# Optimization experiments

Hardware: AMD Instinct MI355X
Metric: run time of the kernel (lower is better)

The kernel has to match this reference:

```python
import jax, jax.numpy as jnp
import numpy as np

N_NODES = 50000
N_EDGES = 1000000
D = 66
NEG_SLOPE = 0.2
EPS_BN = 1e-5


def _glorot(key, shape):
    fan = sum(shape)
    lim = jnp.sqrt(6.0 / fan)
    return jax.random.uniform(key, shape, jnp.float32, -lim, lim)


def setup_inputs() -> dict:
    key = jax.random.key(0)
    ks = jax.random.split(key, 40)
    inp = {
        'h': jax.random.normal(ks[0], (N_NODES, D), jnp.float32),
        'edge_index': jax.random.randint(ks[1], (2, N_EDGES), 0, N_NODES, jnp.int32),
        'edge_weight': jax.random.uniform(ks[2], (N_EDGES, 1), jnp.float32),
        'bn_gamma': jnp.ones((D,), jnp.float32),
        'bn_beta': jnp.zeros((D,), jnp.float32),
    }
    i = 3
    for l in (1, 2, 3):
        inp[f'W{l}'] = _glorot(ks[i], (D, D)); i += 1
        inp[f'b{l}'] = jnp.zeros((D,), jnp.float32)
        inp[f'att_src{l}'] = _glorot(ks[i], (D,)); i += 1
        inp[f'att_dst{l}'] = _glorot(ks[i], (D,)); i += 1
        inp[f'We{l}'] = _glorot(ks[i], (1, D)); i += 1
        inp[f'att_e{l}'] = _glorot(ks[i], (D,)); i += 1
    dims = [(D, D), (D, D), (D, D), (D, D), (D, 22)]
    for l, (din, dout) in enumerate(dims, start=1):
        inp[f'fc{l}_w'] = _glorot(ks[i], (din, dout)); i += 1
        inp[f'fc{l}_b'] = jnp.zeros((dout,), jnp.float32)
    return inp


def _gat_conv(h, src, dst, edge_weight, W, b, att_src, att_dst, We, att_e):
    x = h @ W                                     # [N, D]
    a_src = x @ att_src                           # [N]
    a_dst = x @ att_dst                           # [N]
    a_e = (edge_weight @ We) @ att_e              # [E]
    alpha = a_src[src] + a_dst[dst] + a_e         # [E]
    alpha = jnp.where(alpha > 0, alpha, NEG_SLOPE * alpha)
    # scatter-softmax over destination nodes
    m = jax.ops.segment_max(alpha, dst, num_segments=N_NODES)
    m = jnp.where(jnp.isfinite(m), m, 0.0)
    ex = jnp.exp(alpha - m[dst])
    denom = jax.ops.segment_sum(ex, dst, num_segments=N_NODES)
    coef = ex / (denom[dst] + 1e-16)              # [E]
    out = jax.ops.segment_sum(coef[:, None] * x[src], dst, num_segments=N_NODES)
    return out + b


def reference(h, edge_index, edge_weight, bn_gamma, bn_beta,
              W1, b1, att_src1, att_dst1, We1, att_e1,
              W2, b2, att_src2, att_dst2, We2, att_e2,
              W3, b3, att_src3, att_dst3, We3, att_e3,
              fc1_w, fc1_b, fc2_w, fc2_b, fc3_w, fc3_b,
              fc4_w, fc4_b, fc5_w, fc5_b):
    src, dst = edge_index[0], edge_index[1]
    # BatchNorm1d (training-mode batch statistics, biased variance)
    mean = h.mean(0)
    var = ((h - mean) ** 2).mean(0)
    x = (h - mean) * jax.lax.rsqrt(var + EPS_BN) * bn_gamma + bn_beta
    x = jax.nn.relu(_gat_conv(x, src, dst, edge_weight, W1, b1, att_src1, att_dst1, We1, att_e1))
    x = jax.nn.relu(_gat_conv(x, src, dst, edge_weight, W2, b2, att_src2, att_dst2, We2, att_e2))
    x = jax.nn.relu(_gat_conv(x, src, dst, edge_weight, W3, b3, att_src3, att_dst3, We3, att_e3))
    x = jax.nn.relu(x @ fc1_w + fc1_b)
    x = jax.nn.relu(x @ fc2_w + fc2_b)
    x = jax.nn.relu(x @ fc3_w + fc3_b)
    x = jax.nn.relu(x @ fc4_w + fc4_b)
    return x @ fc5_w + fc5_b
```

## Files before the change

kernel.cpp:

```cpp
#include <hip/hip_runtime.h>
#include <math.h>

#define D 66
#define SP 68
#define NEG_SLOPE 0.2f
#define CAP 6144

typedef short s8v __attribute__((ext_vector_type(8)));
typedef float f4v __attribute__((ext_vector_type(4)));

__device__ __forceinline__ float lrelu(float a){ return a > 0.f ? a : NEG_SLOPE * a; }
__device__ __forceinline__ void fma4(float4& a, float s, const float4& w){
  a.x = fmaf(s, w.x, a.x); a.y = fmaf(s, w.y, a.y);
  a.z = fmaf(s, w.z, a.z); a.w = fmaf(s, w.w, a.w);
}
__device__ __forceinline__ unsigned short bf16r(float f){
  unsigned u = __float_as_uint(f);
  u += 0x7FFFu + ((u >> 16) & 1u);
  return (unsigned short)(u >> 16);
}
__device__ __forceinline__ float bf16f(unsigned short b){
  return __uint_as_float(((unsigned)b) << 16);
}
__device__ __forceinline__ void split8d(const float* p, s8v& a0, s8v& a1){
  #pragma unroll
  for (int j = 0; j < 8; j++){
    float v = p[j];
    unsigned u0 = __float_as_uint(v) & 0xFFFF0000u;
    float r1 = v - __uint_as_float(u0);
    a0[j] = (short)(u0 >> 16);
    a1[j] = (short)(__float_as_uint(r1) >> 16);
  }
}
#define MM4(acc, a0, a1, b0v, b1v)                                         \
  acc = __builtin_amdgcn_mfma_f32_16x16x32_bf16(a0, b0v, acc, 0, 0, 0);    \
  acc = __builtin_amdgcn_mfma_f32_16x16x32_bf16(a1, b0v, acc, 0, 0, 0);    \
  acc = __builtin_amdgcn_mfma_f32_16x16x32_bf16(a0, b1v, acc, 0, 0, 0);    \
  acc = __builtin_amdgcn_mfma_f32_16x16x32_bf16(a1, b1v, acc, 0, 0, 0);

__global__ __launch_bounds__(256) void k_stats_hist(const float* __restrict__ h, const int* __restrict__ dst,
                                                    float* __restrict__ sums, int* __restrict__ bhist,
                                                    int n, int E){
  int t = threadIdx.x;
  if (blockIdx.x < 256){
    __shared__ float ls[2 * D];
    if (t < 2 * D) ls[t] = 0.f;
    __syncthreads();
    int rpb = (n + 255) / 256;
    int r0 = blockIdx.x * rpb;
    int r1 = min(n, r0 + rpb);
    if (t < 3 * D){
      int c = t % D, seg = t / D;
      float s1 = 0.f, s2 = 0.f;
      for (int r = r0 + seg; r < r1; r += 3){
        float v = h[(size_t)r * D + c];
        s1 += v; s2 += v * v;
      }
      atomicAdd(&ls[c], s1);
      atomicAdd(&ls[D + c], s2);
    }
    __syncthreads();
    if (t < 2 * D) atomicAdd(&sums[t], ls[t]);
  } else {
    __shared__ int hh[256];
    hh[t] = 0;
    __syncthreads();
    int stride = 256 * 256;
    for (int e = (blockIdx.x - 256) * 256 + t; e < E; e += stride)
      atomicAdd(&hh[dst[e] >> 8], 1);
    __syncthreads();
    if (hh[t]) atomicAdd(&bhist[t], hh[t]);
  }
}

struct PrepArgs {
  const float *sums, *gamma, *beta;
  const float *We[3], *ae[3];
  const float *gw[3];
  const float *fw[5], *fb[5];
  float *misc; short *W0, *W1; short *F0, *F1; float *bpack;
  int n;
};

__global__ __launch_bounds__(256) void k_prep(PrepArgs pa){
  int t = threadIdx.x;
  if (blockIdx.x == 0){
    if (t < D){
      float mean = pa.sums[t] / (float)pa.n;
      float var  = pa.sums[D + t] / (float)pa.n - mean * mean;
      float inv  = rsqrtf(var + 1e-5f);
      float sc = pa.gamma[t] * inv;
      pa.misc[t] = sc;
      pa.misc[D + t] = pa.beta[t] - mean * sc;
    } else if (t >= D && t < D + 3){
      int l = t - D;
      float c = 0.f;
      for (int d = 0; d < D; d++) c += pa.We[l][d] * pa.ae[l][d];
      pa.misc[2 * D + l] = c;
    }
  } else if (blockIdx.x <= 12){
    int tid = (blockIdx.x - 1) * 256 + t;
    if (tid >= 3 * 960) return;
    int L = tid & 63;
    int ct = (tid >> 6) % 15;
    int lay = tid / 960;
    const float* w = pa.gw[lay];
    int c = ct / 5, tt = ct % 5;
    int nn = tt * 16 + (L & 15);
    int kb = c * 32 + (L >> 4) * 8;
    #pragma unroll
    for (int j = 0; j < 8; j++){
      int k = kb + j;
      float v = (k < D && nn < D) ? w[k * D + nn] : 0.f;
      unsigned short b0 = bf16r(v);
      float r1 = v - bf16f(b0);
      unsigned short b1 = bf16r(r1);
      pa.W0[tid * 8 + j] = (short)b0;
      pa.W1[tid * 8 + j] = (short)b1;
    }
  } else {
    int tid = (blockIdx.x - 13) * 256 + t;
    if (tid < 5 * 960){
      int L = tid & 63;
      int ct = (tid >> 6) % 15;
      int lay = tid / 960;
      const float* w = pa.fw[lay];
      int ncol = (lay == 4) ? 22 : D;
      int c = ct / 5, tt = ct % 5;
      int nn = tt * 16 + (L & 15);
      int kb = c * 32 + (L >> 4) * 8;
      #pragma unroll
      for (int j = 0; j < 8; j++){
        int k = kb + j;
        float v = (k < D && nn < ncol) ? w[k * ncol + nn] : 0.f;
        unsigned short b0 = bf16r(v);
        float r1 = v - bf16f(b0);
        unsigned short b1 = bf16r(r1);
        pa.F0[tid * 8 + j] = (short)b0;
        pa.F1[tid * 8 + j] = (short)b1;
      }
    } else if (tid < 5 * 960 + 400){
      int i = tid - 5 * 960;
      int lay = i / 80, col = i % 80;
      int ncol = (lay == 4) ? 22 : D;
      pa.bpack[i] = (col < ncol) ? pa.fb[lay][col] : 0.f;
    }
  }
}

__global__ void k_bscan(const int* __restrict__ bhist, int* __restrict__ bbase,
                        int* __restrict__ gcur, int* __restrict__ rowptr, int N, int E){
  __shared__ int sh[256];
  int t = threadIdx.x;
  int v = bhist[t];
  sh[t] = v; __syncthreads();
  for (int o = 1; o < 256; o <<= 1){
    int u = (t >= o) ? sh[t - o] : 0;
    __syncthreads();
    sh[t] += u;
    __syncthreads();
  }
  int ex = sh[t] - v;
  bbase[t] = ex;
  gcur[t] = ex;
  if (t == 255){ bbase[256] = sh[255]; rowptr[N] = E; }
}

#define PCHUNK 4096
__global__ __launch_bounds__(256) void k_part(const int* __restrict__ src, const int* __restrict__ dst,
                                              const float* __restrict__ ew,
                                              int* __restrict__ gcur, int2* __restrict__ tmp, int E){
  __shared__ int hist[256];
  __shared__ int base[256];
  int t = threadIdx.x;
  int e0 = blockIdx.x * PCHUNK;
  int eend = min(E, e0 + PCHUNK);
  hist[t] = 0;
  __syncthreads();
  for (int e = e0 + t; e < eend; e += 256)
    atomicAdd(&hist[dst[e] >> 8], 1);
  __syncthreads();
  if (hist[t] > 0) base[t] = atomicAdd(&gcur[t], hist[t]);
  hist[t] = 0;
  __syncthreads();
  for (int e = e0 + t; e < eend; e += 256){
    int d = dst[e];
    int b = d >> 8;
    int off = atomicAdd(&hist[b], 1);
    tmp[base[b] + off] = make_int2((src[e] & 0xffff) | ((d & 255) << 16), __float_as_int(ew[e]));
  }
}

__global__ __launch_bounds__(256) void k_bsort(const int2* __restrict__ tmp, const int* __restrict__ bbase,
                                               int2* __restrict__ epair, int* __restrict__ rowptr, int N){
  __shared__ int2 ebuf[CAP];
  __shared__ int lcnt[256];
  __shared__ int sc[256];
  __shared__ int lcur[256];
  int b = blockIdx.x, t = threadIdx.x;
  int s0 = bbase[b], s1 = bbase[b + 1];
  int cnt = s1 - s0;
  lcnt[t] = 0;
  __syncthreads();
  for (int j = t; j < cnt; j += 256){
    int2 e = tmp[s0 + j];
    if (j < CAP) ebuf[j] = e;
    atomicAdd(&lcnt[(e.x >> 16) & 255], 1);
  }
  __syncthreads();
  int v = lcnt[t];
  sc[t] = v; __syncthreads();
  for (int o = 1; o < 256; o <<= 1){
    int u = (t >= o) ? sc[t - o] : 0;
    __syncthreads();
    sc[t] += u;
    __syncthreads();
  }
  int ex = sc[t] - v;
  int node = (b << 8) + t;
  if (node < N) rowptr[node] = s0 + ex;
  lcur[t] = ex;
  __syncthreads();
  for (int j = t; j < cnt; j += 256){
    int2 e = (j < CAP) ? ebuf[j] : tmp[s0 + j];
    int i = (e.x >> 16) & 255;
    int p = atomicAdd(&lcur[i], 1);
    epair[s0 + p] = make_int2(e.x & 0xffff, e.y);
  }
}

template<bool BN_IN>
__global__ __launch_bounds__(256) void k_mm(const float* __restrict__ X,
    const short* __restrict__ W0, const short* __restrict__ W1,
    const float* __restrict__ att_s, const float* __restrict__ att_d,
    const float* __restrict__ bn,
    float* __restrict__ Y, float* __restrict__ a_src, float* __restrict__ a_dst, int n){
  const int wv = threadIdx.x >> 6, L = threadIdx.x & 63;
  const int quad = L >> 4, m = L & 15;
  const int row0 = blockIdx.x * 64 + wv * 16;
  const int lrow = min(row0 + m, n - 1);
  f4v acc[5];
  #pragma unroll
  for (int t = 0; t < 5; t++) acc[t] = (f4v){0.f,0.f,0.f,0.f};

  #pragma unroll
  for (int c = 0; c < 3; c++){
    float xv[8];
    if (c < 2){
      if (BN_IN){
        const float* hr = X + (size_t)lrow * D + c * 32 + quad * 8;
        #pragma unroll
        for (int j = 0; j < 8; j += 2){
          float2 hv = *(const float2*)(hr + j);
          int col = c * 32 + quad * 8 + j;
          xv[j]     = hv.x * bn[col]     + bn[D + col];
          xv[j + 1] = hv.y * bn[col + 1] + bn[D + col + 1];
        }
      } else {
        const float* xr = X + (size_t)lrow * SP;
        float4 p0 = *(const float4*)&xr[c * 32 + quad * 8];
        float4 p1 = *(const float4*)&xr[c * 32 + quad * 8 + 4];
        xv[0] = p0.x; xv[1] = p0.y; xv[2] = p0.z; xv[3] = p0.w;
        xv[4] = p1.x; xv[5] = p1.y; xv[6] = p1.z; xv[7] = p1.w;
      }
    } else {
      #pragma unroll
      for (int j = 0; j < 8; j++) xv[j] = 0.f;
      if (quad == 0){
        if (BN_IN){
          float2 hv = *(const float2*)(X + (size_t)lrow * D + 64);
          xv[0] = hv.x * bn[64] + bn[D + 64];
          xv[1] = hv.y * bn[65] + bn[D + 65];
        } else {
          float4 p0 = *(const float4*)&X[(size_t)lrow * SP + 64];
          xv[0] = p0.x; xv[1] = p0.y; xv[2] = p0.z; xv[3] = p0.w;
        }
      }
    }
    s8v a0, a1;
    split8d(xv, a0, a1);
    const short* b0p = W0 + (c * 5) * 512 + L * 8;
    const short* b1p = W1 + (c * 5) * 512 + L * 8;
    #pragma unroll
    for (int t = 0; t < 5; t++){
      s8v b0v = *(const s8v*)(b0p + t * 512);
      s8v b1v = *(const s8v*)(b1p + t * 512);
      MM4(acc[t], a0, a1, b0v, b1v)
    }
  }

  float ps[4] = {0.f,0.f,0.f,0.f}, pd[4] = {0.f,0.f,0.f,0.f};
  #pragma unroll
  for (int t = 0; t < 5; t++){
    int col = t * 16 + m;
    float as_v = 0.f, ad_v = 0.f;
    if (col < D){ as_v = att_s[col]; ad_v = att_d[col]; }
    #pragma unroll
    for (int r = 0; r < 4; r++){
      ps[r] += acc[t][r] * as_v;
      pd[r] += acc[t][r] * ad_v;
    }
  }
  #pragma unroll
  for (int r = 0; r < 4; r++){
    int rw = row0 + quad * 4 + r;
    if (rw < n){
      float* yr = Y + (size_t)rw * SP;
      #pragma unroll
      for (int t = 0; t < 4; t++) yr[t * 16 + m] = acc[t][r];
      if (m < 4) yr[64 + m] = (m < 2) ? acc[4][r] : 0.f;
    }
  }
  #pragma unroll
  for (int o = 1; o <= 8; o <<= 1){
    #pragma unroll
    for (int r = 0; r < 4; r++){
      ps[r] += __shfl_xor(ps[r], o);
      pd[r] += __shfl_xor(pd[r], o);
    }
  }
  if (m == 0){
    #pragma unroll
    for (int r = 0; r < 4; r++){
      int rw = row0 + quad * 4 + r;
      if (rw < n){ a_src[rw] = ps[r]; a_dst[rw] = pd[r]; }
    }
  }
}

#define FST 84
__global__ __launch_bounds__(256) void k_fcmm(const float* __restrict__ X,
    const short* __restrict__ W0, const short* __restrict__ W1,
    const float* __restrict__ bpack, float* __restrict__ out, int n){
  __shared__ __align__(16) float xs[2][16][FST];
  const int wv = threadIdx.x >> 6, L = threadIdx.x & 63;
  const int quad = L >> 4, m = L & 15;
  const int rg = wv >> 1, th = wv & 1;
  const int row0 = blockIdx.x * 32 + rg * 16;
  const int lrow = min(row0 + m, n - 1);
  const float* xr = X + (size_t)lrow * SP;

  for (int l = 0; l < 5; l++){
    const int t0 = (l == 4) ? th : (th ? 3 : 0);
    const int nt = (l == 4) ? 1  : (th ? 2 : 3);
    f4v acc[3];
    #pragma unroll
    for (int t = 0; t < 3; t++) acc[t] = (f4v){0.f,0.f,0.f,0.f};
    #pragma unroll
    for (int c = 0; c < 3; c++){
      float xv[8];
      if (l == 0){
        if (c < 2){
          float4 p0 = *(const float4*)&xr[c * 32 + quad * 8];
          float4 p1 = *(const float4*)&xr[c * 32 + quad * 8 + 4];
          xv[0] = p0.x; xv[1] = p0.y; xv[2] = p0.z; xv[3] = p0.w;
          xv[4] = p1.x; xv[5] = p1.y; xv[6] = p1.z; xv[7] = p1.w;
        } else {
          float4 p0 = make_float4(0.f, 0.f, 0.f, 0.f);
          if (quad == 0) p0 = *(const float4*)&xr[64];
          xv[0] = p0.x; xv[1] = p0.y; xv[2] = p0.z; xv[3] = p0.w;
          xv[4] = 0.f; xv[5] = 0.f; xv[6] = 0.f; xv[7] = 0.f;
        }
      } else {
        if (c == 2 && quad >= 2){
          #pragma unroll
          for (int j = 0; j < 8; j++) xv[j] = 0.f;
        } else {
          float4 p0 = *(const float4*)&xs[rg][m][c * 32 + quad * 8];
          float4 p1 = *(const float4*)&xs[rg][m][c * 32 + quad * 8 + 4];
          xv[0] = p0.x; xv[1] = p0.y; xv[2] = p0.z; xv[3] = p0.w;
          xv[4] = p1.x; xv[5] = p1.y; xv[6] = p1.z; xv[7] = p1.w;
        }
      }
      s8v a0, a1;
      split8d(xv, a0, a1);
      const short* b0p = W0 + ((l * 3 + c) * 5 + t0) * 512 + L * 8;
      const short* b1p = W1 + ((l * 3 + c) * 5 + t0) * 512 + L * 8;
      for (int t = 0; t < nt; t++){
        s8v b0v = *(const s8v*)(b0p + t * 512);
        s8v b1v = *(const s8v*)(b1p + t * 512);
        MM4(acc[t], a0, a1, b0v, b1v)
      }
    }
    if (l < 4){
      __syncthreads();
      for (int t = 0; t < nt; t++){
        int col = (t0 + t) * 16 + m;
        float bv = bpack[l * 80 + col];
        #pragma unroll
        for (int r = 0; r < 4; r++){
          float v = acc[t][r] + bv;
          xs[rg][quad * 4 + r][col] = v > 0.f ? v : 0.f;
        }
      }
      __syncthreads();
    } else {
      int col = t0 * 16 + m;
      #pragma unroll
      for (int r = 0; r < 4; r++){
        int rw = row0 + quad * 4 + r;
        if (col < 22 && rw < n) out[(size_t)rw * 22 + col] = acc[0][r] + bpack[4 * 80 + col];
      }
    }
  }
}

__global__ __launch_bounds__(256) void k_agg(const float* __restrict__ y,
                                             const float* __restrict__ a_src, const float* __restrict__ a_dst,
                                             const int* __restrict__ rowptr, const int2* __restrict__ epair,
                                             const float* __restrict__ misc, int cidx,
                                             const float* __restrict__ bias,
                                             float* __restrict__ xout, int n){
  const int wave = (int)((blockIdx.x * (size_t)blockDim.x + threadIdx.x) >> 6);
  const int lane = threadIdx.x & 63;
  const int half = lane >> 5, l32 = lane & 31;
  const int node = wave * 2 + half;
  const bool valid = node < n;
  const int nd = valid ? node : (n - 1);
  const int beg = rowptr[nd];
  const int deg = rowptr[nd + 1] - beg;
  const float ce  = misc[2 * D + cidx];
  const float adn = a_dst[nd];
  const int dmax = max(deg, __shfl_xor(deg, 32));

  const int g = l32 >> 2, q = l32 & 3;
  float4 acc0 = make_float4(0.f,0.f,0.f,0.f);
  float4 acc1 = make_float4(0.f,0.f,0.f,0.f);
  float4 acc2 = make_float4(0.f,0.f,0.f,0.f);
  float4 acc3 = make_float4(0.f,0.f,0.f,0.f);
  float2 tacc = make_float2(0.f,0.f);

  if (dmax <= 32){
    int s = 0; float coef = 0.f;
    float al = -INFINITY;
    if (l32 < deg){
      int2 ep = epair[beg + l32];
      s = ep.x;
      al = lrelu(a_src[s] + adn + ce * __int_as_float(ep.y));
    }
    float mx = al;
    #pragma unroll
    for (int o = 16; o; o >>= 1) mx = fmaxf(mx, __shfl_xor(mx, o));
    float ex = (l32 < deg) ? __expf(al - mx) : 0.f;
    float sum = ex;
    #pragma unroll
    for (int o = 16; o; o >>= 1) sum += __shfl_xor(sum, o);
    float inv = 1.f / (sum + 1e-16f);
    coef = ex * inv;

    int   stv[4];
    float ctv[4];
    #pragma unroll
    for (int i = 0; i < 4; i++){
      int lsrc = (lane & 32) | (8 * i + g);
      stv[i] = __shfl(s,    lsrc);
      ctv[i] = __shfl(coef, lsrc);
    }
    #pragma unroll
    for (int i = 0; i < 4; i++){
      if (8 * i + g < deg){
        const float* row = y + (size_t)stv[i] * SP;
        fma4(acc0, ctv[i], *(const float4*)&row[      4 * q]);
        fma4(acc1, ctv[i], *(const float4*)&row[16 + 4 * q]);
        fma4(acc2, ctv[i], *(const float4*)&row[32 + 4 * q]);
        fma4(acc3, ctv[i], *(const float4*)&row[48 + 4 * q]);
        if (q == 0){
          float2 tv = *(const float2*)&row[64];
          tacc.x += ctv[i] * tv.x; tacc.y += ctv[i] * tv.y;
        }
      }
    }
  } else {
    float mx = -INFINITY;
    for (int j0 = 0; j0 < dmax; j0 += 32){
      int j = j0 + l32;
      if (j < deg){
        int2 ep = epair[beg + j];
        mx = fmaxf(mx, lrelu(a_src[ep.x] + adn + ce * __int_as_float(ep.y)));
      }
    }
    #pragma unroll
    for (int o = 16; o; o >>= 1) mx = fmaxf(mx, __shfl_xor(mx, o));
    float sum = 0.f;
    for (int j0 = 0; j0 < dmax; j0 += 32){
      int j = j0 + l32;
      if (j < deg){
        int2 ep = epair[beg + j];
        sum += __expf(lrelu(a_src[ep.x] + adn + ce * __int_as_float(ep.y)) - mx);
      }
    }
    #pragma unroll
    for (int o = 16; o; o >>= 1) sum += __shfl_xor(sum, o);
    float inv = 1.f / (sum + 1e-16f);

    for (int j0 = 0; j0 < dmax; j0 += 32){
      int cs = 0; float cc = 0.f;
      int j = j0 + l32;
      if (j < deg){
        int2 ep = epair[beg + j];
        cs = ep.x;
        cc = __expf(lrelu(a_src[cs] + adn + ce * __int_as_float(ep.y)) - mx) * inv;
      }
      int   stv[4];
      float ctv[4];
      #pragma unroll
      for (int i = 0; i < 4; i++){
        int lsrc = (lane & 32) | (8 * i + g);
        stv[i] = __shfl(cs, lsrc);
        ctv[i] = __shfl(cc, lsrc);
      }
      int cmax = min(32, dmax - j0);
      #pragma unroll
      for (int i = 0; i < 4; i++){
        int e = 8 * i + g;
        if (j0 + e < deg && e < cmax){
          const float* row = y + (size_t)stv[i] * SP;
          fma4(acc0, ctv[i], *(const float4*)&row[      4 * q]);
          fma4(acc1, ctv[i], *(const float4*)&row[16 + 4 * q]);
          fma4(acc2, ctv[i], *(const float4*)&row[32 + 4 * q]);
          fma4(acc3, ctv[i], *(const float4*)&row[48 + 4 * q]);
          if (q == 0){
            float2 tv = *(const float2*)&row[64];
            tacc.x += ctv[i] * tv.x; tacc.y += ctv[i] * tv.y;
          }
        }
      }
    }
  }

  #pragma unroll
  for (int o = 4; o <= 16; o <<= 1){
    acc0.x += __shfl_xor(acc0.x, o); acc0.y += __shfl_xor(acc0.y, o);
    acc0.z += __shfl_xor(acc0.z, o); acc0.w += __shfl_xor(acc0.w, o);
    acc1.x += __shfl_xor(acc1.x, o); acc1.y += __shfl_xor(acc1.y, o);
    acc1.z += __shfl_xor(acc1.z, o); acc1.w += __shfl_xor(acc1.w, o);
    acc2.x += __shfl_xor(acc2.x, o); acc2.y += __shfl_xor(acc2.y, o);
    acc2.z += __shfl_xor(acc2.z, o); acc2.w += __shfl_xor(acc2.w, o);
    acc3.x += __shfl_xor(acc3.x, o); acc3.y += __shfl_xor(acc3.y, o);
    acc3.z += __shfl_xor(acc3.z, o); acc3.w += __shfl_xor(acc3.w, o);
    tacc.x += __shfl_xor(tacc.x, o); tacc.y += __shfl_xor(tacc.y, o);
  }
  if (valid){
    float* orow = xout + (size_t)node * SP;
    if (l32 < 4){
      int c0 = 4 * l32;
      float4 v;
      v.x = acc0.x + bias[c0+0]; v.x = v.x > 0.f ? v.x : 0.f;
      v.y = acc0.y + bias[c0+1]; v.y = v.y > 0.f ? v.y : 0.f;
      v.z = acc0.z + bias[c0+2]; v.z = v.z > 0.f ? v.z : 0.f;
      v.w = acc0.w + bias[c0+3]; v.w = v.w > 0.f ? v.w : 0.f;
      *(float4*)&orow[c0] = v;
      v.x = acc1.x + bias[16+c0+0]; v.x = v.x > 0.f ? v.x : 0.f;
      v.y = acc1.y + bias[16+c0+1]; v.y = v.y > 0.f ? v.y : 0.f;
      v.z = acc1.z + bias[16+c0+2]; v.z = v.z > 0.f ? v.z : 0.f;
      v.w = acc1.w + bias[16+c0+3]; v.w = v.w > 0.f ? v.w : 0.f;
      *(float4*)&orow[16 + c0] = v;
      v.x = acc2.x + bias[32+c0+0]; v.x = v.x > 0.f ? v.x : 0.f;
      v.y = acc2.y + bias[32+c0+1]; v.y = v.y > 0.f ? v.y : 0.f;
      v.z = acc2.z + bias[32+c0+2]; v.z = v.z > 0.f ? v.z : 0.f;
      v.w = acc2.w + bias[32+c0+3]; v.w = v.w > 0.f ? v.w : 0.f;
      *(float4*)&orow[32 + c0] = v;
      v.x = acc3.x + bias[48+c0+0]; v.x = v.x > 0.f ? v.x : 0.f;
      v.y = acc3.y + bias[48+c0+1]; v.y = v.y > 0.f ? v.y : 0.f;
      v.z = acc3.z + bias[48+c0+2]; v.z = v.z > 0.f ? v.z : 0.f;
      v.w = acc3.w + bias[48+c0+3]; v.w = v.w > 0.f ? v.w : 0.f;
      *(float4*)&orow[48 + c0] = v;
    }
    if (l32 == 0){
      float4 tv;
      tv.x = tacc.x + bias[64]; tv.x = tv.x > 0.f ? tv.x : 0.f;
      tv.y = tacc.y + bias[65]; tv.y = tv.y > 0.f ? tv.y : 0.f;
      tv.z = 0.f; tv.w = 0.f;
      *(float4*)&orow[64] = tv;
    }
  }
}

extern "C" void kernel_launch(void* const* d_in, const int* in_sizes, int n_in,
                              void* d_out, int out_size, void* d_ws, size_t ws_size,
                              hipStream_t stream){
  const float* h     = (const float*)d_in[0];
  const int*   ei    = (const int*)  d_in[1];
  const float* ew    = (const float*)d_in[2];
  const float* gamma = (const float*)d_in[3];
  const float* beta  = (const float*)d_in[4];
  const float *Wl[3], *bl[3], *asl[3], *adl[3], *Wel[3], *ael[3];
  int idx = 5;
  for (int l = 0; l < 3; l++){
    Wl[l]  = (const float*)d_in[idx++];
    bl[l]  = (const float*)d_in[idx++];
    asl[l] = (const float*)d_in[idx++];
    adl[l] = (const float*)d_in[idx++];
    Wel[l] = (const float*)d_in[idx++];
    ael[l] = (const float*)d_in[idx++];
  }
  const float *fw[5], *fb[5];
  for (int l = 0; l < 5; l++){ fw[l] = (const float*)d_in[idx++]; fb[l] = (const float*)d_in[idx++]; }

  int N = in_sizes[0] / D;
  int E = in_sizes[1] / 2;
  const int* src  = ei;
  const int* dstp = ei + E;

  char* base = (char*)d_ws;
  size_t o = 0;
  auto alloc = [&](size_t b){ size_t r = o; o += (b + 255) & ~(size_t)255; return r; };
  float*  bufA   = (float*)(base + alloc((size_t)N * SP * 4));
  float*  bufB   = (float*)(base + alloc((size_t)N * SP * 4));
  float*  a_src  = (float*)(base + alloc((size_t)N * 4));
  float*  a_dst  = (float*)(base + alloc((size_t)N * 4));
  float*  misc   = (float*)(base + alloc(512 * 4));
  float*  sums   = (float*)(base + alloc(2 * D * 4));
  int*    rowptr = (int*)  (base + alloc((size_t)(N + 1) * 4));
  int*    bhist  = (int*)  (base + alloc(256 * 4));
  int*    bbase  = (int*)  (base + alloc(257 * 4));
  int*    gcur   = (int*)  (base + alloc(256 * 4));
  int2*   epair  = (int2*) (base + alloc((size_t)E * 8));
  short*  W0p    = (short*)(base + alloc(3 * 7680 * 2));
  short*  W1p    = (short*)(base + alloc(3 * 7680 * 2));
  short*  FW0p   = (short*)(base + alloc(5 * 7680 * 2));
  short*  FW1p   = (short*)(base + alloc(5 * 7680 * 2));
  float*  bpack  = (float*)(base + alloc(400 * 4));
  int2*   tmp    = (int2*)bufB;

  hipMemsetAsync(sums, 0, 2 * D * 4, stream);
  hipMemsetAsync(bhist, 0, 256 * 4, stream);

  k_stats_hist<<<512, 256, 0, stream>>>(h, dstp, sums, bhist, N, E);

  PrepArgs pa;
  pa.sums = sums; pa.gamma = gamma; pa.beta = beta;
  for (int l = 0; l < 3; l++){ pa.We[l] = Wel[l]; pa.ae[l] = ael[l]; pa.gw[l] = Wl[l]; }
  for (int l = 0; l < 5; l++){ pa.fw[l] = fw[l]; pa.fb[l] = fb[l]; }
  pa.misc = misc; pa.W0 = W0p; pa.W1 = W1p;
  pa.F0 = FW0p; pa.F1 = FW1p; pa.bpack = bpack; pa.n = N;
  k_prep<<<34, 256, 0, stream>>>(pa);

  int NB = (N + 255) >> 8;
  k_bscan<<<1, 256, 0, stream>>>(bhist, bbase, gcur, rowptr, N, E);
  k_part<<<(E + PCHUNK - 1) / PCHUNK, 256, 0, stream>>>(src, dstp, ew, gcur, tmp, E);
  k_bsort<<<NB, 256, 0, stream>>>(tmp, bbase, epair, rowptr, N);

  int gb = (N + 63) / 64;
  int ab = (N + 7) / 8;

  k_mm<true ><<<gb, 256, 0, stream>>>(h,    W0p + 0 * 7680, W1p + 0 * 7680,
                                      asl[0], adl[0], misc, bufB, a_src, a_dst, N);
  k_agg<<<ab, 256, 0, stream>>>(bufB, a_src, a_dst, rowptr, epair, misc, 0, bl[0], bufA, N);
  k_mm<false><<<gb, 256, 0, stream>>>(bufA, W0p + 1 * 7680, W1p + 1 * 7680,
                                      asl[1], adl[1], misc, bufB, a_src, a_dst, N);
  k_agg<<<ab, 256, 0, stream>>>(bufB, a_src, a_dst, rowptr, epair, misc, 1, bl[1], bufA, N);
  k_mm<false><<<gb, 256, 0, stream>>>(bufA, W0p + 2 * 7680, W1p + 2 * 7680,
                                      asl[2], adl[2], misc, bufB, a_src, a_dst, N);
  k_agg<<<ab, 256, 0, stream>>>(bufB, a_src, a_dst, rowptr, epair, misc, 2, bl[2], bufA, N);

  int gb2 = (N + 31) / 32;
  k_fcmm<<<gb2, 256, 0, stream>>>(bufA, FW0p, FW1p, bpack, (float*)d_out, N);
}
```

Before: 420.4 us.

## Split node features into 64-wide rows plus packed tail/attention float4

Node feature rows shrink from a 68-float stride to a 64-float stride (256 bytes, aligned). Columns 64-65 move into a separate float4 per node, which also carries a_src and a_dst. In the aggregation kernel, one float4 gather per edge now supplies the attention score and both tail columns. This removes the separate a_src/a_dst loads and the odd tail reads from the feature row. The cost is an extra shuffle reduction for the tail accumulator and one more side buffer that must be written and read.

```diff
diff --git a/kernel.cpp b/kernel.cpp
--- a/kernel.cpp
+++ b/kernel.cpp
@@ -2,7 +2,7 @@
 #include <math.h>
 
 #define D 66
-#define SP 68
+#define YR 64
 #define NEG_SLOPE 0.2f
 #define CAP 6144
 
@@ -230,11 +230,11 @@
 }
 
 template<bool BN_IN>
-__global__ __launch_bounds__(256) void k_mm(const float* __restrict__ X,
+__global__ __launch_bounds__(256) void k_mm(const float* __restrict__ X, const float4* __restrict__ Xt,
     const short* __restrict__ W0, const short* __restrict__ W1,
     const float* __restrict__ att_s, const float* __restrict__ att_d,
     const float* __restrict__ bn,
-    float* __restrict__ Y, float* __restrict__ a_src, float* __restrict__ a_dst, int n){
+    float* __restrict__ Y, float4* __restrict__ Yt, int n){
   const int wv = threadIdx.x >> 6, L = threadIdx.x & 63;
   const int quad = L >> 4, m = L & 15;
   const int row0 = blockIdx.x * 64 + wv * 16;
@@ -257,7 +257,7 @@
           xv[j + 1] = hv.y * bn[col + 1] + bn[D + col + 1];
         }
       } else {
-        const float* xr = X + (size_t)lrow * SP;
+        const float* xr = X + (size_t)lrow * YR;
         float4 p0 = *(const float4*)&xr[c * 32 + quad * 8];
         float4 p1 = *(const float4*)&xr[c * 32 + quad * 8 + 4];
         xv[0] = p0.x; xv[1] = p0.y; xv[2] = p0.z; xv[3] = p0.w;
@@ -272,8 +272,8 @@
           xv[0] = hv.x * bn[64] + bn[D + 64];
           xv[1] = hv.y * bn[65] + bn[D + 65];
         } else {
-          float4 p0 = *(const float4*)&X[(size_t)lrow * SP + 64];
-          xv[0] = p0.x; xv[1] = p0.y; xv[2] = p0.z; xv[3] = p0.w;
+          float4 t = Xt[lrow];
+          xv[0] = t.x; xv[1] = t.y;
         }
       }
     }
@@ -305,12 +305,14 @@
   for (int r = 0; r < 4; r++){
     int rw = row0 + quad * 4 + r;
     if (rw < n){
-      float* yr = Y + (size_t)rw * SP;
+      float* yr = Y + (size_t)rw * YR;
       #pragma unroll
       for (int t = 0; t < 4; t++) yr[t * 16 + m] = acc[t][r];
-      if (m < 4) yr[64 + m] = (m < 2) ? acc[4][r] : 0.f;
-    }
-  }
+    }
+  }
+  float c65[4];
+  #pragma unroll
+  for (int r = 0; r < 4; r++) c65[r] = __shfl_down(acc[4][r], 1);
   #pragma unroll
   for (int o = 1; o <= 8; o <<= 1){
     #pragma unroll
@@ -323,13 +325,13 @@
     #pragma unroll
     for (int r = 0; r < 4; r++){
       int rw = row0 + quad * 4 + r;
-      if (rw < n){ a_src[rw] = ps[r]; a_dst[rw] = pd[r]; }
+      if (rw < n) Yt[rw] = make_float4(acc[4][r], c65[r], ps[r], pd[r]);
     }
   }
 }
 
 #define FST 84
-__global__ __launch_bounds__(256) void k_fcmm(const float* __restrict__ X,
+__global__ __launch_bounds__(256) void k_fcmm(const float* __restrict__ X, const float4* __restrict__ Xt,
     const short* __restrict__ W0, const short* __restrict__ W1,
     const float* __restrict__ bpack, float* __restrict__ out, int n){
   __shared__ __align__(16) float xs[2][16][FST];
@@ -338,7 +340,7 @@
   const int rg = wv >> 1, th = wv & 1;
   const int row0 = blockIdx.x * 32 + rg * 16;
   const int lrow = min(row0 + m, n - 1);
-  const float* xr = X + (size_t)lrow * SP;
+  const float* xr = X + (size_t)lrow * YR;
 
   for (int l = 0; l < 5; l++){
     const int t0 = (l == 4) ? th : (th ? 3 : 0);
@@ -356,10 +358,12 @@
           xv[0] = p0.x; xv[1] = p0.y; xv[2] = p0.z; xv[3] = p0.w;
           xv[4] = p1.x; xv[5] = p1.y; xv[6] = p1.z; xv[7] = p1.w;
         } else {
-          float4 p0 = make_float4(0.f, 0.f, 0.f, 0.f);
-          if (quad == 0) p0 = *(const float4*)&xr[64];
-          xv[0] = p0.x; xv[1] = p0.y; xv[2] = p0.z; xv[3] = p0.w;
-          xv[4] = 0.f; xv[5] = 0.f; xv[6] = 0.f; xv[7] = 0.f;
+          #pragma unroll
+          for (int j = 0; j < 8; j++) xv[j] = 0.f;
+          if (quad == 0){
+            float4 t = Xt[lrow];
+            xv[0] = t.x; xv[1] = t.y;
+          }
         }
       } else {
         if (c == 2 && quad >= 2){
@@ -405,12 +409,11 @@
   }
 }
 
-__global__ __launch_bounds__(256) void k_agg(const float* __restrict__ y,
-                                             const float* __restrict__ a_src, const float* __restrict__ a_dst,
+__global__ __launch_bounds__(256) void k_agg(const float* __restrict__ y, const float4* __restrict__ yt,
                                              const int* __restrict__ rowptr, const int2* __restrict__ epair,
                                              const float* __restrict__ misc, int cidx,
                                              const float* __restrict__ bias,
-                                             float* __restrict__ xout, int n){
+                                             float* __restrict__ xout, float4* __restrict__ xt, int n){
   const int wave = (int)((blockIdx.x * (size_t)blockDim.x + threadIdx.x) >> 6);
   const int lane = threadIdx.x & 63;
   const int half = lane >> 5, l32 = lane & 31;
@@ -420,7 +423,7 @@
   const int beg = rowptr[nd];
   const int deg = rowptr[nd + 1] - beg;
   const float ce  = misc[2 * D + cidx];
-  const float adn = a_dst[nd];
+  const float adn = yt[nd].w;
   const int dmax = max(deg, __shfl_xor(deg, 32));
 
   const int g = l32 >> 2, q = l32 & 3;
@@ -433,10 +436,12 @@
   if (dmax <= 32){
     int s = 0; float coef = 0.f;
     float al = -INFINITY;
+    float4 ytv = make_float4(0.f,0.f,0.f,0.f);
     if (l32 < deg){
       int2 ep = epair[beg + l32];
       s = ep.x;
-      al = lrelu(a_src[s] + adn + ce * __int_as_float(ep.y));
+      ytv = yt[s];
+      al = lrelu(ytv.z + adn + ce * __int_as_float(ep.y));
     }
     float mx = al;
     #pragma unroll
@@ -447,6 +452,8 @@
     for (int o = 16; o; o >>= 1) sum += __shfl_xor(sum, o);
     float inv = 1.f / (sum + 1e-16f);
     coef = ex * inv;
+    tacc.x = coef * ytv.x;
+    tacc.y = coef * ytv.y;
 
     int   stv[4];
     float ctv[4];
@@ -459,15 +466,11 @@
     #pragma unroll
     for (int i = 0; i < 4; i++){
       if (8 * i + g < deg){
-        const float* row = y + (size_t)stv[i] * SP;
+        const float* row = y + (size_t)stv[i] * YR;
         fma4(acc0, ctv[i], *(const float4*)&row[      4 * q]);
         fma4(acc1, ctv[i], *(const float4*)&row[16 + 4 * q]);
         fma4(acc2, ctv[i], *(const float4*)&row[32 + 4 * q]);
         fma4(acc3, ctv[i], *(const float4*)&row[48 + 4 * q]);
-        if (q == 0){
-          float2 tv = *(const float2*)&row[64];
-          tacc.x += ctv[i] * tv.x; tacc.y += ctv[i] * tv.y;
-        }
       }
     }
   } else {
@@ -476,7 +479,7 @@
       int j = j0 + l32;
       if (j < deg){
         int2 ep = epair[beg + j];
-        mx = fmaxf(mx, lrelu(a_src[ep.x] + adn + ce * __int_as_float(ep.y)));
+        mx = fmaxf(mx, lrelu(yt[ep.x].z + adn + ce * __int_as_float(ep.y)));
       }
     }
     #pragma unroll
@@ -486,7 +489,7 @@
       int j = j0 + l32;
       if (j < deg){
         int2 ep = epair[beg + j];
-        sum += __expf(lrelu(a_src[ep.x] + adn + ce * __int_as_float(ep.y)) - mx);
+        sum += __expf(lrelu(yt[ep.x].z + adn + ce * __int_as_float(ep.y)) - mx);
       }
     }
     #pragma unroll
@@ -499,7 +502,10 @@
       if (j < deg){
         int2 ep = epair[beg + j];
         cs = ep.x;
-        cc = __expf(lrelu(a_src[cs] + adn + ce * __int_as_float(ep.y)) - mx) * inv;
+        float4 yv = yt[cs];
+        cc = __expf(lrelu(yv.z + adn + ce * __int_as_float(ep.y)) - mx) * inv;
+        tacc.x += cc * yv.x;
+        tacc.y += cc * yv.y;
       }
       int   stv[4];
       float ctv[4];
@@ -514,20 +520,18 @@
       for (int i = 0; i < 4; i++){
         int e = 8 * i + g;
         if (j0 + e < deg && e < cmax){
-          const float* row = y + (size_t)stv[i] * SP;
+          const float* row = y + (size_t)stv[i] * YR;
           fma4(acc0, ctv[i], *(const float4*)&row[      4 * q]);
           fma4(acc1, ctv[i], *(const float4*)&row[16 + 4 * q]);
           fma4(acc2, ctv[i], *(const float4*)&row[32 + 4 * q]);
           fma4(acc3, ctv[i], *(const float4*)&row[48 + 4 * q]);
-          if (q == 0){
-            float2 tv = *(const float2*)&row[64];
-            tacc.x += ctv[i] * tv.x; tacc.y += ctv[i] * tv.y;
-          }
         }
       }
     }
   }
 
+  tacc.x += __shfl_xor(tacc.x, 1); tacc.y += __shfl_xor(tacc.y, 1);
+  tacc.x += __shfl_xor(tacc.x, 2); tacc.y += __shfl_xor(tacc.y, 2);
   #pragma unroll
   for (int o = 4; o <= 16; o <<= 1){
     acc0.x += __shfl_xor(acc0.x, o); acc0.y += __shfl_xor(acc0.y, o);
@@ -541,7 +545,7 @@
     tacc.x += __shfl_xor(tacc.x, o); tacc.y += __shfl_xor(tacc.y, o);
   }
   if (valid){
-    float* orow = xout + (size_t)node * SP;
+    float* orow = xout + (size_t)node * YR;
     if (l32 < 4){
       int c0 = 4 * l32;
       float4 v;
@@ -567,11 +571,9 @@
       *(float4*)&orow[48 + c0] = v;
     }
     if (l32 == 0){
-      float4 tv;
-      tv.x = tacc.x + bias[64]; tv.x = tv.x > 0.f ? tv.x : 0.f;
-      tv.y = tacc.y + bias[65]; tv.y = tv.y > 0.f ? tv.y : 0.f;
-      tv.z = 0.f; tv.w = 0.f;
-      *(float4*)&orow[64] = tv;
+      float tx = tacc.x + bias[64]; tx = tx > 0.f ? tx : 0.f;
+      float ty = tacc.y + bias[65]; ty = ty > 0.f ? ty : 0.f;
+      xt[node] = make_float4(tx, ty, 0.f, 0.f);
     }
   }
 }
@@ -605,10 +607,10 @@
   char* base = (char*)d_ws;
   size_t o = 0;
   auto alloc = [&](size_t b){ size_t r = o; o += (b + 255) & ~(size_t)255; return r; };
-  float*  bufA   = (float*)(base + alloc((size_t)N * SP * 4));
-  float*  bufB   = (float*)(base + alloc((size_t)N * SP * 4));
-  float*  a_src  = (float*)(base + alloc((size_t)N * 4));
-  float*  a_dst  = (float*)(base + alloc((size_t)N * 4));
+  float*  bufA   = (float*)(base + alloc((size_t)N * YR * 4));
+  float*  bufB   = (float*)(base + alloc((size_t)N * YR * 4));
+  float4* tA     = (float4*)(base + alloc((size_t)N * 16));
+  float4* tB     = (float4*)(base + alloc((size_t)N * 16));
   float*  misc   = (float*)(base + alloc(512 * 4));
   float*  sums   = (float*)(base + alloc(2 * D * 4));
   int*    rowptr = (int*)  (base + alloc((size_t)(N + 1) * 4));
@@ -644,16 +646,16 @@
   int gb = (N + 63) / 64;
   int ab = (N + 7) / 8;
 
-  k_mm<true ><<<gb, 256, 0, stream>>>(h,    W0p + 0 * 7680, W1p + 0 * 7680,
-                                      asl[0], adl[0], misc, bufB, a_src, a_dst, N);
-  k_agg<<<ab, 256, 0, stream>>>(bufB, a_src, a_dst, rowptr, epair, misc, 0, bl[0], bufA, N);
-  k_mm<false><<<gb, 256, 0, stream>>>(bufA, W0p + 1 * 7680, W1p + 1 * 7680,
-                                      asl[1], adl[1], misc, bufB, a_src, a_dst, N);
-  k_agg<<<ab, 256, 0, stream>>>(bufB, a_src, a_dst, rowptr, epair, misc, 1, bl[1], bufA, N);
-  k_mm<false><<<gb, 256, 0, stream>>>(bufA, W0p + 2 * 7680, W1p + 2 * 7680,
-                                      asl[2], adl[2], misc, bufB, a_src, a_dst, N);
-  k_agg<<<ab, 256, 0, stream>>>(bufB, a_src, a_dst, rowptr, epair, misc, 2, bl[2], bufA, N);
+  k_mm<true ><<<gb, 256, 0, stream>>>(h,    nullptr, W0p + 0 * 7680, W1p + 0 * 7680,
+                                      asl[0], adl[0], misc, bufB, tB, N);
+  k_agg<<<ab, 256, 0, stream>>>(bufB, tB, rowptr, epair, misc, 0, bl[0], bufA, tA, N);
+  k_mm<false><<<gb, 256, 0, stream>>>(bufA, tA, W0p + 1 * 7680, W1p + 1 * 7680,
+                                      asl[1], adl[1], misc, bufB, tB, N);
+  k_agg<<<ab, 256, 0, stream>>>(bufB, tB, rowptr, epair, misc, 1, bl[1], bufA, tA, N);
+  k_mm<false><<<gb, 256, 0, stream>>>(bufA, tA, W0p + 2 * 7680, W1p + 2 * 7680,
+                                      asl[2], adl[2], misc, bufB, tB, N);
+  k_agg<<<ab, 256, 0, stream>>>(bufB, tB, rowptr, epair, misc, 2, bl[2], bufA, tA, N);
 
   int gb2 = (N + 31) / 32;
-  k_fcmm<<<gb2, 256, 0, stream>>>(bufA, FW0p, FW1p, bpack, (float*)d_out, N);
-}
+  k_fcmm<<<gb2, 256, 0, stream>>>(bufA, tA, FW0p, FW1p, bpack, (float*)d_out, N);
+}
```

Result: faster. 395.9 us (median of 2 runs) (-5.8%).
